# Performance work log

Measured on AMD Instinct MI355X. Metric: run time of the kernel, lower is better.

The kernel has to match this reference:

```python
import jax, jax.numpy as jnp
import numpy as np
from jax import lax

TOPK = 5
MAX_CANDIDATES = 32
MAX_LAG_CAP = 168


def setup_inputs() -> dict:
    key = jax.random.key(0)
    x = jax.random.normal(key, (32, 4096, 512), dtype=jnp.float32)
    return {"x": x}


def reference(x):
    B, L, D = x.shape
    x_mean = x.mean(axis=-1)                          # [B, L]
    max_lag = min(L - 1, MAX_LAG_CAP)
    num = min(max_lag, MAX_CANDIDATES)
    # torch.linspace(..., dtype=long) truncates toward zero; astype does too
    lags = jnp.linspace(1.0, float(max_lag), num).astype(jnp.int32)  # [num]

    t = jnp.arange(L)

    def score_for_lag(lag):
        # (x_mean[:, :-lag] * x_mean[:, lag:]).mean(1), via masked circular shift
        shifted = jnp.roll(x_mean, -lag, axis=1)       # x_mean[:, t+lag] (wrapped)
        mask = (t < (L - lag)).astype(x_mean.dtype)    # [L]
        return (x_mean * shifted * mask).sum(axis=1) / (L - lag).astype(x_mean.dtype)

    scores = jax.vmap(score_for_lag, out_axes=1)(lags)  # [B, num]

    k = min(TOPK, num)
    vals, idx = lax.top_k(scores, k)                    # [B, k]
    sel_lags = lags[idx]                                # [B, k] int
    weights = vals / (vals.sum(axis=1, keepdims=True) + 1e-6)  # [B, k]

    roll_batch = jax.vmap(lambda xb, lag: jnp.roll(xb, lag, axis=0))

    out = jnp.zeros_like(x)
    for j in range(k):  # small fixed k
        rolled = roll_batch(x, sel_lags[:, j])          # [B, L, D]
        out = out + weights[:, j, None, None] * rolled
    return out
```

## Files before the change

### kernel.cpp

```cpp
#include <hip/hip_runtime.h>

#define BB 32
#define LL 4096
#define DD 512
#define NUM 32
#define KK 5

typedef float f32x4 __attribute__((ext_vector_type(4)));

__device__ __constant__ int d_LAGS[NUM] = {
    1, 6, 11, 17, 22, 27, 33, 38, 44, 49, 54, 60, 65, 71, 76, 81,
    87, 92, 97, 103, 108, 114, 119, 124, 130, 135, 141, 146, 151, 157, 162, 168};

__global__ __launch_bounds__(256) void k_mean(const float* __restrict__ x,
                                              float* __restrict__ xm) {
    int row  = blockIdx.x * 4 + (threadIdx.x >> 6);
    int lane = threadIdx.x & 63;
    const float* p = x + (size_t)row * DD;
    f32x4 a = *reinterpret_cast<const f32x4*>(p + 4 * lane);
    f32x4 b = *reinterpret_cast<const f32x4*>(p + 4 * lane + 256);
    float s = (a.x + a.y) + (a.z + a.w) + (b.x + b.y) + (b.z + b.w);
#pragma unroll
    for (int off = 32; off > 0; off >>= 1) s += __shfl_down(s, off, 64);
    if (lane == 0) xm[row] = s * (1.0f / DD);
}

__global__ __launch_bounds__(256) void k_scores_topk(const float* __restrict__ xm,
                                                     float* __restrict__ w,
                                                     int* __restrict__ sel) {
    __shared__ float row[LL];
    __shared__ float sc[NUM];
    int b = blockIdx.x;
    for (int i = threadIdx.x; i < LL; i += 256) row[i] = xm[b * LL + i];
    __syncthreads();

    int wid = threadIdx.x >> 6, lane = threadIdx.x & 63;
#pragma unroll
    for (int q = 0; q < 8; ++q) {
        int k   = q * 4 + wid;
        int lag = d_LAGS[k];
        int n   = LL - lag;
        float s = 0.0f;
        for (int t = lane; t < n; t += 64) s += row[t] * row[t + lag];
#pragma unroll
        for (int off = 32; off > 0; off >>= 1) s += __shfl_down(s, off, 64);
        if (lane == 0) sc[k] = s / (float)n;
    }
    __syncthreads();

    if (threadIdx.x == 0) {
        float v[NUM];
#pragma unroll
        for (int i = 0; i < NUM; i++) v[i] = sc[i];
        float vals[KK];
        int   idx[KK];
#pragma unroll
        for (int j = 0; j < KK; j++) {
            float best = -INFINITY;
            int bi = 0;
#pragma unroll
            for (int i = 0; i < NUM; i++) {
                if (v[i] > best) { best = v[i]; bi = i; }
            }
            vals[j] = best;
            idx[j]  = bi;
            v[bi]   = -INFINITY;
        }
        float sum = 0.0f;
#pragma unroll
        for (int j = 0; j < KK; j++) sum += vals[j];
        float den = sum + 1e-6f;
#pragma unroll
        for (int j = 0; j < KK; j++) {
            w[b * KK + j]   = vals[j] / den;
            sel[b * KK + j] = d_LAGS[idx[j]];
        }
    }
}

__global__ __launch_bounds__(512) void k_combine(const float* __restrict__ x,
                                                 const float* __restrict__ w,
                                                 const int* __restrict__ sel,
                                                 float* __restrict__ out) {
    unsigned bid = blockIdx.x;
    const unsigned QUADS_PER_XCD = (BB * LL / 4) / 8;
    unsigned qid = (bid & 7u) * QUADS_PER_XCD + (bid >> 3);
    unsigned r   = qid * 4 + (threadIdx.x >> 7);
    int b = (int)(r >> 12);
    int t = (int)(r & 4095u);

    float ww[KK];
    int   lg[KK];
#pragma unroll
    for (int j = 0; j < KK; j++) {
        ww[j] = w[b * KK + j];
        lg[j] = sel[b * KK + j];
    }

    const float* xb = x + (size_t)b * (LL * DD);
    int d4 = threadIdx.x & 127;
    f32x4 acc = {0.f, 0.f, 0.f, 0.f};
#pragma unroll
    for (int j = 0; j < KK; j++) {
        int src = (t - lg[j]) & (LL - 1);
        f32x4 v = *reinterpret_cast<const f32x4*>(xb + (size_t)src * DD + 4 * d4);
        float wj = ww[j];
        acc.x += wj * v.x;
        acc.y += wj * v.y;
        acc.z += wj * v.z;
        acc.w += wj * v.w;
    }
    __builtin_nontemporal_store(acc,
        reinterpret_cast<f32x4*>(out + (size_t)r * DD + 4 * d4));
}

extern "C" void kernel_launch(void* const* d_in, const int* in_sizes, int n_in,
                              void* d_out, int out_size, void* d_ws, size_t ws_size,
                              hipStream_t stream) {
    const float* x = (const float*)d_in[0];
    float* out = (float*)d_out;

    char* ws = (char*)d_ws;
    float* xm  = (float*)(ws);
    float* wts = (float*)(ws + (size_t)BB * LL * 4);
    int*   sel = (int*)  (ws + (size_t)BB * LL * 4 + BB * KK * 4);

    k_mean<<<(BB * LL) / 4, 256, 0, stream>>>(x, xm);
    k_scores_topk<<<BB, 256, 0, stream>>>(xm, wts, sel);
    k_combine<<<(BB * LL) / 4, 512, 0, stream>>>(x, wts, sel, out);
}
```

Measured before the change: 155.7 us.

## Fuse mean, scores, top-k and combine into one cooperative kernel with per-batch barriers

Replaces the three separate launches with one cooperative kernel of 1024 blocks. Each batch is handled by a group of 32 blocks pinned to one XCD, and the groups synchronise through atomic-counter barriers between the mean, score, top-k and combine phases. The lag scores are now spread across blocks, one lag per block, instead of one block per batch. The aim is to remove launch gaps and the serial single-block score stage, and to keep each batch's data in the same XCD's L2 cache for the combine reads. The trade-off is spin-wait barriers, an extra init launch, and a residency requirement that all 1024 blocks run at once.

```diff
diff --git a/kernel.cpp b/kernel.cpp
--- a/kernel.cpp
+++ b/kernel.cpp
@@ -5,6 +5,9 @@
 #define DD 512
 #define NUM 32
 #define KK 5
+#define GRID 1024
+#define GPB 32
+#define NGRP 32
 
 typedef float f32x4 __attribute__((ext_vector_type(4)));
 
@@ -12,46 +15,84 @@
     1, 6, 11, 17, 22, 27, 33, 38, 44, 49, 54, 60, 65, 71, 76, 81,
     87, 92, 97, 103, 108, 114, 119, 124, 130, 135, 141, 146, 151, 157, 162, 168};
 
-__global__ __launch_bounds__(256) void k_mean(const float* __restrict__ x,
-                                              float* __restrict__ xm) {
-    int row  = blockIdx.x * 4 + (threadIdx.x >> 6);
-    int lane = threadIdx.x & 63;
-    const float* p = x + (size_t)row * DD;
-    f32x4 a = *reinterpret_cast<const f32x4*>(p + 4 * lane);
-    f32x4 b = *reinterpret_cast<const f32x4*>(p + 4 * lane + 256);
-    float s = (a.x + a.y) + (a.z + a.w) + (b.x + b.y) + (b.z + b.w);
-#pragma unroll
-    for (int off = 32; off > 0; off >>= 1) s += __shfl_down(s, off, 64);
-    if (lane == 0) xm[row] = s * (1.0f / DD);
+__global__ __launch_bounds__(96) void k_init(int* __restrict__ ctrs) {
+    ctrs[threadIdx.x] = 0;
 }
 
-__global__ __launch_bounds__(256) void k_scores_topk(const float* __restrict__ xm,
-                                                     float* __restrict__ w,
-                                                     int* __restrict__ sel) {
-    __shared__ float row[LL];
-    __shared__ float sc[NUM];
-    int b = blockIdx.x;
-    for (int i = threadIdx.x; i < LL; i += 256) row[i] = xm[b * LL + i];
+__device__ __forceinline__ void group_barrier(int* ctr) {
     __syncthreads();
+    if (threadIdx.x == 0) {
+        __threadfence();
+        atomicAdd(ctr, 1);
+        while (__hip_atomic_load(ctr, __ATOMIC_ACQUIRE, __HIP_MEMORY_SCOPE_AGENT) < GPB) {
+            __builtin_amdgcn_s_sleep(2);
+        }
+        __threadfence();
+    }
+    __syncthreads();
+}
 
-    int wid = threadIdx.x >> 6, lane = threadIdx.x & 63;
+__global__ __launch_bounds__(256, 4) void k_fused(const float* __restrict__ x,
+                                                  float* __restrict__ xm,
+                                                  float* __restrict__ scores,
+                                                  float* __restrict__ wts,
+                                                  int* __restrict__ sel,
+                                                  float* __restrict__ out,
+                                                  int* __restrict__ ctrs) {
+    const int bid   = blockIdx.x;
+    const int xcd   = bid & 7;
+    const int slot  = bid >> 3;
+    const int gi    = slot >> 5;
+    const int rank  = slot & 31;
+    const int batch = xcd * 4 + gi;
+
+    int* ctrA = ctrs + batch;
+    int* ctrB = ctrs + NGRP + batch;
+    int* ctrC = ctrs + 2 * NGRP + batch;
+
+    const int tid  = threadIdx.x;
+    const int wid  = tid >> 6;
+    const int lane = tid & 63;
+
+    {
+        const int wv = rank * 4 + wid;
+        const float* xb = x + (size_t)batch * (LL * DD);
+        float* xmb = xm + batch * LL;
+        for (int i = 0; i < 32; ++i) {
+            int row = wv * 32 + i;
+            const float* p = xb + (size_t)row * DD;
+            f32x4 a = *reinterpret_cast<const f32x4*>(p + 4 * lane);
+            f32x4 b = *reinterpret_cast<const f32x4*>(p + 4 * lane + 256);
+            float s = (a.x + a.y) + (a.z + a.w) + (b.x + b.y) + (b.z + b.w);
 #pragma unroll
-    for (int q = 0; q < 8; ++q) {
-        int k   = q * 4 + wid;
-        int lag = d_LAGS[k];
-        int n   = LL - lag;
+            for (int off = 32; off > 0; off >>= 1) s += __shfl_down(s, off, 64);
+            if (lane == 0) xmb[row] = s * (1.0f / DD);
+        }
+    }
+    group_barrier(ctrA);
+
+    {
+        int lag = d_LAGS[rank];
+        const float* row = xm + batch * LL;
+        int n = LL - lag;
         float s = 0.0f;
-        for (int t = lane; t < n; t += 64) s += row[t] * row[t + lag];
+        for (int t = tid; t < n; t += 256) s += row[t] * row[t + lag];
 #pragma unroll
         for (int off = 32; off > 0; off >>= 1) s += __shfl_down(s, off, 64);
-        if (lane == 0) sc[k] = s / (float)n;
+        __shared__ float red[4];
+        if (lane == 0) red[wid] = s;
+        __syncthreads();
+        if (tid == 0) {
+            float tot = (red[0] + red[1]) + (red[2] + red[3]);
+            scores[batch * NUM + rank] = tot / (float)n;
+        }
     }
-    __syncthreads();
+    group_barrier(ctrB);
 
-    if (threadIdx.x == 0) {
+    if (rank == 0 && tid == 0) {
         float v[NUM];
 #pragma unroll
-        for (int i = 0; i < NUM; i++) v[i] = sc[i];
+        for (int i = 0; i < NUM; i++) v[i] = scores[batch * NUM + i];
         float vals[KK];
         int   idx[KK];
 #pragma unroll
@@ -72,46 +113,42 @@
         float den = sum + 1e-6f;
 #pragma unroll
         for (int j = 0; j < KK; j++) {
-            w[b * KK + j]   = vals[j] / den;
-            sel[b * KK + j] = d_LAGS[idx[j]];
+            wts[batch * KK + j] = vals[j] / den;
+            sel[batch * KK + j] = d_LAGS[idx[j]];
         }
     }
-}
+    group_barrier(ctrC);
 
-__global__ __launch_bounds__(512) void k_combine(const float* __restrict__ x,
-                                                 const float* __restrict__ w,
-                                                 const int* __restrict__ sel,
-                                                 float* __restrict__ out) {
-    unsigned bid = blockIdx.x;
-    const unsigned QUADS_PER_XCD = (BB * LL / 4) / 8;
-    unsigned qid = (bid & 7u) * QUADS_PER_XCD + (bid >> 3);
-    unsigned r   = qid * 4 + (threadIdx.x >> 7);
-    int b = (int)(r >> 12);
-    int t = (int)(r & 4095u);
-
-    float ww[KK];
-    int   lg[KK];
+    {
+        float ww[KK];
+        int   lg[KK];
 #pragma unroll
-    for (int j = 0; j < KK; j++) {
-        ww[j] = w[b * KK + j];
-        lg[j] = sel[b * KK + j];
+        for (int j = 0; j < KK; j++) {
+            ww[j] = wts[batch * KK + j];
+            lg[j] = sel[batch * KK + j];
+        }
+        const float* xb = x + (size_t)batch * (LL * DD);
+        float* ob = out + (size_t)batch * (LL * DD);
+        const int half = tid >> 7;
+        const int d4   = tid & 127;
+        for (int i = 0; i < 64; ++i) {
+            int p  = i * 32 + rank;
+            int lt = p * 2 + half;
+            f32x4 acc = {0.f, 0.f, 0.f, 0.f};
+#pragma unroll
+            for (int j = 0; j < KK; j++) {
+                int src = (lt - lg[j]) & (LL - 1);
+                f32x4 v = *reinterpret_cast<const f32x4*>(xb + (size_t)src * DD + 4 * d4);
+                float wj = ww[j];
+                acc.x += wj * v.x;
+                acc.y += wj * v.y;
+                acc.z += wj * v.z;
+                acc.w += wj * v.w;
+            }
+            __builtin_nontemporal_store(acc,
+                reinterpret_cast<f32x4*>(ob + (size_t)lt * DD + 4 * d4));
+        }
     }
-
-    const float* xb = x + (size_t)b * (LL * DD);
-    int d4 = threadIdx.x & 127;
-    f32x4 acc = {0.f, 0.f, 0.f, 0.f};
-#pragma unroll
-    for (int j = 0; j < KK; j++) {
-        int src = (t - lg[j]) & (LL - 1);
-        f32x4 v = *reinterpret_cast<const f32x4*>(xb + (size_t)src * DD + 4 * d4);
-        float wj = ww[j];
-        acc.x += wj * v.x;
-        acc.y += wj * v.y;
-        acc.z += wj * v.z;
-        acc.w += wj * v.w;
-    }
-    __builtin_nontemporal_store(acc,
-        reinterpret_cast<f32x4*>(out + (size_t)r * DD + 4 * d4));
 }
 
 extern "C" void kernel_launch(void* const* d_in, const int* in_sizes, int n_in,
@@ -121,11 +158,16 @@
     float* out = (float*)d_out;
 
     char* ws = (char*)d_ws;
-    float* xm  = (float*)(ws);
-    float* wts = (float*)(ws + (size_t)BB * LL * 4);
-    int*   sel = (int*)  (ws + (size_t)BB * LL * 4 + BB * KK * 4);
+    int*   ctrs   = (int*)ws;
+    float* xm     = (float*)(ws + 1024);
+    float* scores = (float*)(ws + 1024 + (size_t)BB * LL * 4);
+    float* wts    = (float*)(ws + 1024 + (size_t)BB * LL * 4 + BB * NUM * 4);
+    int*   sel    = (int*)(ws + 1024 + (size_t)BB * LL * 4 + BB * NUM * 4 + BB * KK * 4);
 
-    k_mean<<<(BB * LL) / 4, 256, 0, stream>>>(x, xm);
-    k_scores_topk<<<BB, 256, 0, stream>>>(xm, wts, sel);
-    k_combine<<<(BB * LL) / 4, 512, 0, stream>>>(x, wts, sel, out);
+    k_init<<<1, 96, 0, stream>>>(ctrs);
+
+    void* args[] = {(void*)&x, (void*)&xm, (void*)&scores, (void*)&wts,
+                    (void*)&sel, (void*)&out, (void*)&ctrs};
+    hipLaunchCooperativeKernel((const void*)k_fused, dim3(GRID), dim3(256),
+                               args, 0, stream);
 }
```

New measurement: 429.9 us. 176% more time.
